# Kernel optimization log

Measured on AMD Instinct MI355X. Metric: run time of the kernel, lower is better.

The kernel has to match this reference:

```python
import jax, jax.numpy as jnp
import numpy as np
from jax.scipy.special import logsumexp

B, F, V, C, K, KP = 8192, 32, 64, 32, 8, 7  # batch, features, values/feature, classes, gate options, padded pair candidates
TEMP = 1.0
EPS = 1e-06


def _structure():
    # candidate 0 = self table; candidates 1..7 = pair tables conditioned on preceding features
    mask = np.zeros((F - 1, K), dtype=bool)
    mask[:, 0] = True
    cond = np.zeros((F - 1, KP), dtype=np.int32)
    for i in range(F - 1):
        fi = i + 1
        for j in range(min(fi, KP)):
            mask[i, j + 1] = True
            cond[i, j] = fi - 1 - j
    return jnp.asarray(cond), jnp.asarray(mask)


def setup_inputs() -> dict:
    key = jax.random.key(0)
    ks = jax.random.split(key, 6)
    cond_index, valid_mask = _structure()
    return {
        "x": jax.random.randint(ks[0], (B, F), 0, V, dtype=jnp.int32),
        "training": True,
        "class_logits": jax.random.normal(ks[1], (C,), jnp.float32) * 0.1,
        "table0": jax.random.normal(ks[2], (V, C), jnp.float32) * 0.1,
        "self_tables": jax.random.normal(ks[3], (F - 1, V, C), jnp.float32) * 0.1,
        "pair_tables": jax.random.normal(ks[4], (F - 1, KP, V, V, C), jnp.float32) * 0.1,
        "structure_logits": jax.random.normal(ks[5], (F - 1, K), jnp.float32) * 0.1,
        "u_noise": jax.random.uniform(jax.random.fold_in(key, 7), (F - 1, K), jnp.float32),
        "cond_index": cond_index,
        "valid_mask": valid_mask,
    }


def reference(x, training, class_logits, table0, self_tables, pair_tables,
              structure_logits, u_noise, cond_index, valid_mask):
    # class prior term
    cl = class_logits - logsumexp(class_logits)  # [C]
    t0 = table0 - logsumexp(table0, axis=0, keepdims=True)  # [V,C]
    out = cl[None, :] + t0[x[:, 0]]  # [B,C]

    # Gumbel-softmax gate over candidate parent sets (training path)
    g = -jnp.log(-jnp.log(u_noise + EPS) + EPS)
    gate_logits = jnp.where(valid_mask, (structure_logits + g) / TEMP, -jnp.inf)
    w = jax.nn.softmax(gate_logits, axis=-1)  # [F-1,K]; padded entries get weight 0

    f_idx = jnp.arange(F - 1)
    xs = x[:, 1:]  # [B,F-1] feature values

    # self (class-only) candidate tables, normalized over the feature-value axis
    st = self_tables - logsumexp(self_tables, axis=1, keepdims=True)  # [F-1,V,C]
    self_g = st[f_idx[None, :], xs]  # [B,F-1,C]
    out = out + jnp.einsum('bfc,f->bc', self_g, w[:, 0])

    # pair candidate tables, normalized over the feature-value axis (axis 2)
    pt = pair_tables - logsumexp(pair_tables, axis=2, keepdims=True)  # [F-1,KP,V,V,C]
    xc = x[:, cond_index]  # [B,F-1,KP] conditioning feature values
    k_idx = jnp.arange(KP)
    pair_g = pt[f_idx[None, :, None], k_idx[None, None, :], xs[:, :, None], xc]  # [B,F-1,KP,C]
    out = out + jnp.einsum('bfkc,fk->bc', pair_g, w[:, 1:])
    return out
```

## Files before the change

### kernel.cpp

```cpp
#include <hip/hip_runtime.h>
#include <math.h>

#define B_  8192
#define F_  32
#define V_  64
#define C_  32
#define KP_ 7
#define EPS_ 1e-6f

#define WS_OFF  256
#define WS_ETAB 288
#define WS_G    512
#define WS_LSE  66048

__device__ const int d_split[9] = {0, 25, 50, 74, 99, 123, 148, 172, 196};

__global__ __launch_bounds__(1024)
void prep_kernel(const float* __restrict__ cl, const float* __restrict__ t0,
                 const float* __restrict__ st, const float* __restrict__ sl,
                 const float* __restrict__ un, float* __restrict__ ws) {
    __shared__ float gl[31][8];
    __shared__ float wsm[31][8];
    __shared__ float lse_self[31][32];
    int tid = threadIdx.x;

    if (tid < 248) {
        int f = tid >> 3, k = tid & 7;
        int kmax = min(f + 1, KP_);
        bool valid = (k <= kmax);
        float u = un[tid];
        float g = -__logf(-__logf(u + EPS_) + EPS_);
        gl[f][k] = valid ? (sl[tid] + g) : -INFINITY;
    }
    if (tid >= 248 && tid < 256) ws[tid] = 0.f;
    if (tid < 200) {
        int q = tid / 25, i = tid % 25;
        int g = d_split[q] + i;
        int packed;
        if (g < d_split[q + 1]) {
            int f = 0, base = 0;
            for (;;) { int cnt = min(f + 1, KP_); if (g < base + cnt) break; base += cnt; f++; }
            int k = g - base;
            packed = ((f * 8 + k + 1) << 20) | ((f * KP_ + k) << 12) | ((f + 1) << 6) | (f - k);
        } else {
            packed = (248 << 20);
        }
        ((int*)ws)[WS_ETAB + tid] = packed;
    }
    __syncthreads();
    if (tid < 248) {
        int f = tid >> 3, k = tid & 7;
        float m = -INFINITY;
        #pragma unroll
        for (int j = 0; j < 8; j++) m = fmaxf(m, gl[f][j]);
        float s = 0.f;
        #pragma unroll
        for (int j = 0; j < 8; j++) s += __expf(gl[f][j] - m);
        float wv = __expf(gl[f][k] - m) / s;
        wsm[f][k] = wv;
        ws[tid] = wv;
    }
    if (tid < 992) {
        int f = tid >> 5, c = tid & 31;
        float s = 0.f;
        #pragma unroll 8
        for (int v = 0; v < V_; v++) s += __expf(st[(f * V_ + v) * C_ + c]);
        lse_self[f][c] = __logf(s);
    }
    __syncthreads();
    if (tid < 32) {
        int c = tid;
        float scl = 0.f;
        #pragma unroll
        for (int j = 0; j < C_; j++) scl += __expf(cl[j]);
        float lse_cl = __logf(scl);
        float s0 = 0.f;
        #pragma unroll 8
        for (int v = 0; v < V_; v++) s0 += __expf(t0[v * C_ + c]);
        float lse_t0 = __logf(s0);
        float acc = cl[c] - lse_cl - lse_t0;
        for (int f = 0; f < 31; f++) acc -= wsm[f][0] * lse_self[f][c];
        ws[WS_OFF + c] = acc;
    }
}

__global__ __launch_bounds__(256)
void lse_kernel(const float* __restrict__ pt, float* __restrict__ ws) {
    int idx = blockIdx.x * 256 + threadIdx.x;
    int c4 = idx & 7, v = (idx >> 3) & 63, fk = idx >> 9;
    const float* p = pt + (size_t)fk * (V_ * V_ * C_) + v * C_ + c4 * 4;
    float4 s = make_float4(0.f, 0.f, 0.f, 0.f);
    for (int a = 0; a < V_; a += 8) {
        float4 l[8];
        #pragma unroll
        for (int i = 0; i < 8; i++)
            l[i] = *(const float4*)(p + (a + i) * (V_ * C_));
        #pragma unroll
        for (int i = 0; i < 8; i++) {
            s.x += __expf(l[i].x); s.y += __expf(l[i].y);
            s.z += __expf(l[i].z); s.w += __expf(l[i].w);
        }
    }
    float4 r;
    r.x = __logf(s.x); r.y = __logf(s.y); r.z = __logf(s.z); r.w = __logf(s.w);
    ((float4*)(ws + WS_LSE))[idx] = r;
}

__global__ __launch_bounds__(256)
void foldg_kernel(const float* __restrict__ t0, const float* __restrict__ st,
                  float* __restrict__ ws) {
    int idx = blockIdx.x * 256 + threadIdx.x;
    int c4 = idx & 7, v = (idx >> 3) & 63, j = idx >> 9;
    int nk = min(KP_, 31 - j);
    const float4* lse4 = (const float4*)(ws + WS_LSE);
    float4 g;
    if (j == 0) {
        g = ((const float4*)t0)[v * 8 + c4];
    } else {
        float w0 = ws[(j - 1) * 8];
        float4 sv = ((const float4*)st)[((j - 1) * V_ + v) * 8 + c4];
        g.x = w0 * sv.x; g.y = w0 * sv.y; g.z = w0 * sv.z; g.w = w0 * sv.w;
    }
    for (int k = 0; k < nk; k++) {
        int f = j + k;
        float wv = ws[f * 8 + k + 1];
        float4 lv = lse4[((f * KP_ + k) * V_ + v) * 8 + c4];
        g.x -= wv * lv.x; g.y -= wv * lv.y; g.z -= wv * lv.z; g.w -= wv * lv.w;
    }
    ((float4*)(ws + WS_G))[idx] = g;
}

__global__ __launch_bounds__(256)
void main_kernel(const int* __restrict__ x, const float* __restrict__ pt,
                 const float* __restrict__ ws, float* __restrict__ out) {
    __shared__ int   xsh[4 * 33];
    __shared__ float wsh[256];
    __shared__ int   etab[200];
    __shared__ float4 offv[8];
    __shared__ float4 part[7][32];
    int tid = threadIdx.x;
    if (tid < 128) xsh[(tid >> 5) * 33 + (tid & 31)] = x[blockIdx.x * 128 + tid];
    wsh[tid] = ws[tid];
    if (tid < 200) etab[tid] = ((const int*)ws)[WS_ETAB + tid];
    if (tid < 8)   offv[tid] = ((const float4*)(ws + WS_OFF))[tid];
    __syncthreads();

    const float4* __restrict__ G4 = (const float4*)(ws + WS_G);
    int q  = tid >> 5;
    int r  = (tid >> 3) & 3;
    int c4 = tid & 7;
    const int* xrow = &xsh[r * 33];
    float4 acc = make_float4(0.f, 0.f, 0.f, 0.f);

    #pragma unroll
    for (int jj = 0; jj < 4; jj++) {
        int j = q * 4 + jj;
        float4 gv = G4[(j * V_ + xrow[j]) * 8 + c4];
        acc.x += gv.x; acc.y += gv.y; acc.z += gv.z; acc.w += gv.w;
    }
    if (q == 0) {
        float4 ov = offv[c4];
        acc.x += ov.x; acc.y += ov.y; acc.z += ov.z; acc.w += ov.w;
    }

    int beg = q * 25;
    #pragma unroll
    for (int ch = 0; ch < 5; ch++) {
        float4 pv[5];
        float  wt[5];
        #pragma unroll
        for (int i = 0; i < 5; i++) {
            int pk = etab[beg + ch * 5 + i];
            int ci = pk & 63, fi = (pk >> 6) & 63;
            int fk = (pk >> 12) & 255, widx = (pk >> 20) & 255;
            int xv = xrow[fi], xc = xrow[ci];
            pv[i] = *(const float4*)(pt + ((size_t)(fk * V_ + xv) * V_ + xc) * C_ + c4 * 4);
            wt[i] = wsh[widx];
        }
        #pragma unroll
        for (int i = 0; i < 5; i++) {
            acc.x += wt[i] * pv[i].x; acc.y += wt[i] * pv[i].y;
            acc.z += wt[i] * pv[i].z; acc.w += wt[i] * pv[i].w;
        }
    }

    if (q > 0) part[q - 1][r * 8 + c4] = acc;
    __syncthreads();
    if (q == 0) {
        #pragma unroll
        for (int p = 0; p < 7; p++) {
            float4 pv = part[p][r * 8 + c4];
            acc.x += pv.x; acc.y += pv.y; acc.z += pv.z; acc.w += pv.w;
        }
        ((float4*)out)[(blockIdx.x * 4 + r) * 8 + c4] = acc;
    }
}

extern "C" void kernel_launch(void* const* d_in, const int* in_sizes, int n_in,
                              void* d_out, int out_size, void* d_ws, size_t ws_size,
                              hipStream_t stream) {
    const int*   x   = (const int*)  d_in[0];
    const float* cl  = (const float*)d_in[2];
    const float* t0  = (const float*)d_in[3];
    const float* st  = (const float*)d_in[4];
    const float* pt  = (const float*)d_in[5];
    const float* sl  = (const float*)d_in[6];
    const float* un  = (const float*)d_in[7];
    float* ws  = (float*)d_ws;
    float* out = (float*)d_out;

    prep_kernel<<<1, 1024, 0, stream>>>(cl, t0, st, sl, un, ws);
    lse_kernel<<<434, 256, 0, stream>>>(pt, ws);
    foldg_kernel<<<64, 256, 0, stream>>>(t0, st, ws);
    main_kernel<<<2048, 256, 0, stream>>>(x, pt, ws, out);
}
```

Baseline: 230.3 us.

## Fuse prep into LSE kernel and gather pair tables from fp16 copy

Merges the single-block prep kernel into the LSE kernel as an extra block, removing one launch and the serial one-block stage. The LSE pass also writes an fp16 copy of the pair tables into workspace, and the main kernel gathers from that copy, halving bytes per random gather. The cost is an extra ~57MB write per call, and fp16 rounding of the table values adds small numerical error. The fp16 path is used only when the workspace is large enough.

```diff
diff --git a/kernel.cpp b/kernel.cpp
--- a/kernel.cpp
+++ b/kernel.cpp
@@ -1,4 +1,5 @@
 #include <hip/hip_runtime.h>
+#include <hip/hip_fp16.h>
 #include <math.h>
 
 #define B_  8192
@@ -12,98 +13,113 @@
 #define WS_ETAB 288
 #define WS_G    512
 #define WS_LSE  66048
+#define WS_H    2097152ull
+#define H_BYTES (217ull * V_ * V_ * C_ * 2ull)
+#define NEED_WS (WS_H * 4ull + H_BYTES)
 
 __device__ const int d_split[9] = {0, 25, 50, 74, 99, 123, 148, 172, 196};
 
-__global__ __launch_bounds__(1024)
-void prep_kernel(const float* __restrict__ cl, const float* __restrict__ t0,
-                 const float* __restrict__ st, const float* __restrict__ sl,
-                 const float* __restrict__ un, float* __restrict__ ws) {
-    __shared__ float gl[31][8];
-    __shared__ float wsm[31][8];
-    __shared__ float lse_self[31][32];
-    int tid = threadIdx.x;
-
-    if (tid < 248) {
-        int f = tid >> 3, k = tid & 7;
-        int kmax = min(f + 1, KP_);
-        bool valid = (k <= kmax);
-        float u = un[tid];
-        float g = -__logf(-__logf(u + EPS_) + EPS_);
-        gl[f][k] = valid ? (sl[tid] + g) : -INFINITY;
-    }
-    if (tid >= 248 && tid < 256) ws[tid] = 0.f;
-    if (tid < 200) {
-        int q = tid / 25, i = tid % 25;
-        int g = d_split[q] + i;
-        int packed;
-        if (g < d_split[q + 1]) {
-            int f = 0, base = 0;
-            for (;;) { int cnt = min(f + 1, KP_); if (g < base + cnt) break; base += cnt; f++; }
-            int k = g - base;
-            packed = ((f * 8 + k + 1) << 20) | ((f * KP_ + k) << 12) | ((f + 1) << 6) | (f - k);
+template<int CVT>
+__global__ __launch_bounds__(256)
+void lse_prep_kernel(const float* __restrict__ pt,
+                     const float* __restrict__ cl, const float* __restrict__ t0,
+                     const float* __restrict__ st, const float* __restrict__ sl,
+                     const float* __restrict__ un, float* __restrict__ ws) {
+    if (blockIdx.x < 434) {
+        int idx = blockIdx.x * 256 + threadIdx.x;
+        int c4 = idx & 7, v = (idx >> 3) & 63, fk = idx >> 9;
+        size_t eoff = (size_t)fk * (V_ * V_ * C_) + v * C_ + c4 * 4;
+        const float* p = pt + eoff;
+        __half* ph = (__half*)(ws + WS_H) + eoff;
+        float4 s = make_float4(0.f, 0.f, 0.f, 0.f);
+        for (int a = 0; a < V_; a += 8) {
+            float4 l[8];
+            #pragma unroll
+            for (int i = 0; i < 8; i++)
+                l[i] = *(const float4*)(p + (size_t)(a + i) * (V_ * C_));
+            if (CVT) {
+                #pragma unroll
+                for (int i = 0; i < 8; i++) {
+                    union { __half2 h; unsigned u; } ha, hb;
+                    ha.h = __floats2half2_rn(l[i].x, l[i].y);
+                    hb.h = __floats2half2_rn(l[i].z, l[i].w);
+                    *(uint2*)(ph + (size_t)(a + i) * (V_ * C_)) = make_uint2(ha.u, hb.u);
+                }
+            }
+            #pragma unroll
+            for (int i = 0; i < 8; i++) {
+                s.x += __expf(l[i].x); s.y += __expf(l[i].y);
+                s.z += __expf(l[i].z); s.w += __expf(l[i].w);
+            }
+        }
+        float4 r;
+        r.x = __logf(s.x); r.y = __logf(s.y); r.z = __logf(s.z); r.w = __logf(s.w);
+        ((float4*)(ws + WS_LSE))[idx] = r;
+    } else {
+        __shared__ float gl[31][8];
+        __shared__ float wsm[31][8];
+        __shared__ float lsf[31][32];
+        int tid = threadIdx.x;
+        if (tid < 248) {
+            int f = tid >> 3, k = tid & 7;
+            int kmax = min(f + 1, KP_);
+            bool valid = (k <= kmax);
+            float u = un[tid];
+            float g = -__logf(-__logf(u + EPS_) + EPS_);
+            gl[f][k] = valid ? (sl[tid] + g) : -INFINITY;
         } else {
-            packed = (248 << 20);
-        }
-        ((int*)ws)[WS_ETAB + tid] = packed;
-    }
-    __syncthreads();
-    if (tid < 248) {
-        int f = tid >> 3, k = tid & 7;
-        float m = -INFINITY;
-        #pragma unroll
-        for (int j = 0; j < 8; j++) m = fmaxf(m, gl[f][j]);
-        float s = 0.f;
-        #pragma unroll
-        for (int j = 0; j < 8; j++) s += __expf(gl[f][j] - m);
-        float wv = __expf(gl[f][k] - m) / s;
-        wsm[f][k] = wv;
-        ws[tid] = wv;
-    }
-    if (tid < 992) {
-        int f = tid >> 5, c = tid & 31;
-        float s = 0.f;
-        #pragma unroll 8
-        for (int v = 0; v < V_; v++) s += __expf(st[(f * V_ + v) * C_ + c]);
-        lse_self[f][c] = __logf(s);
-    }
-    __syncthreads();
-    if (tid < 32) {
-        int c = tid;
-        float scl = 0.f;
-        #pragma unroll
-        for (int j = 0; j < C_; j++) scl += __expf(cl[j]);
-        float lse_cl = __logf(scl);
-        float s0 = 0.f;
-        #pragma unroll 8
-        for (int v = 0; v < V_; v++) s0 += __expf(t0[v * C_ + c]);
-        float lse_t0 = __logf(s0);
-        float acc = cl[c] - lse_cl - lse_t0;
-        for (int f = 0; f < 31; f++) acc -= wsm[f][0] * lse_self[f][c];
-        ws[WS_OFF + c] = acc;
-    }
-}
-
-__global__ __launch_bounds__(256)
-void lse_kernel(const float* __restrict__ pt, float* __restrict__ ws) {
-    int idx = blockIdx.x * 256 + threadIdx.x;
-    int c4 = idx & 7, v = (idx >> 3) & 63, fk = idx >> 9;
-    const float* p = pt + (size_t)fk * (V_ * V_ * C_) + v * C_ + c4 * 4;
-    float4 s = make_float4(0.f, 0.f, 0.f, 0.f);
-    for (int a = 0; a < V_; a += 8) {
-        float4 l[8];
-        #pragma unroll
-        for (int i = 0; i < 8; i++)
-            l[i] = *(const float4*)(p + (a + i) * (V_ * C_));
-        #pragma unroll
-        for (int i = 0; i < 8; i++) {
-            s.x += __expf(l[i].x); s.y += __expf(l[i].y);
-            s.z += __expf(l[i].z); s.w += __expf(l[i].w);
-        }
-    }
-    float4 r;
-    r.x = __logf(s.x); r.y = __logf(s.y); r.z = __logf(s.z); r.w = __logf(s.w);
-    ((float4*)(ws + WS_LSE))[idx] = r;
+            ws[tid] = 0.f;
+        }
+        if (tid < 200) {
+            int q = tid / 25, i = tid % 25;
+            int g = d_split[q] + i;
+            int packed;
+            if (g < d_split[q + 1]) {
+                int f = 0, base = 0;
+                for (;;) { int cnt = min(f + 1, KP_); if (g < base + cnt) break; base += cnt; f++; }
+                int k = g - base;
+                packed = ((f * 8 + k + 1) << 20) | ((f * KP_ + k) << 12) | ((f + 1) << 6) | (f - k);
+            } else {
+                packed = (248 << 20);
+            }
+            ((int*)ws)[WS_ETAB + tid] = packed;
+        }
+        __syncthreads();
+        if (tid < 248) {
+            int f = tid >> 3, k = tid & 7;
+            float m = -INFINITY;
+            #pragma unroll
+            for (int j = 0; j < 8; j++) m = fmaxf(m, gl[f][j]);
+            float s = 0.f;
+            #pragma unroll
+            for (int j = 0; j < 8; j++) s += __expf(gl[f][j] - m);
+            float wv = __expf(gl[f][k] - m) / s;
+            wsm[f][k] = wv;
+            ws[tid] = wv;
+        }
+        for (int i = tid; i < 992; i += 256) {
+            int f = i >> 5, c = i & 31;
+            float s = 0.f;
+            #pragma unroll 8
+            for (int v = 0; v < V_; v++) s += __expf(st[(f * V_ + v) * C_ + c]);
+            lsf[f][c] = __logf(s);
+        }
+        __syncthreads();
+        if (tid < 32) {
+            int c = tid;
+            float scl = 0.f;
+            #pragma unroll
+            for (int j = 0; j < C_; j++) scl += __expf(cl[j]);
+            float lse_cl = __logf(scl);
+            float s0 = 0.f;
+            #pragma unroll 8
+            for (int v = 0; v < V_; v++) s0 += __expf(t0[v * C_ + c]);
+            float lse_t0 = __logf(s0);
+            float acc = cl[c] - lse_cl - lse_t0;
+            for (int f = 0; f < 31; f++) acc -= wsm[f][0] * lsf[f][c];
+            ws[WS_OFF + c] = acc;
+        }
+    }
 }
 
 __global__ __launch_bounds__(256)
@@ -130,6 +146,7 @@
     ((float4*)(ws + WS_G))[idx] = g;
 }
 
+template<int CVT>
 __global__ __launch_bounds__(256)
 void main_kernel(const int* __restrict__ x, const float* __restrict__ pt,
                  const float* __restrict__ ws, float* __restrict__ out) {
@@ -145,7 +162,8 @@
     if (tid < 8)   offv[tid] = ((const float4*)(ws + WS_OFF))[tid];
     __syncthreads();
 
-    const float4* __restrict__ G4 = (const float4*)(ws + WS_G);
+    const float4* __restrict__ G4  = (const float4*)(ws + WS_G);
+    const __half* __restrict__ pth = (const __half*)(ws + WS_H);
     int q  = tid >> 5;
     int r  = (tid >> 3) & 3;
     int c4 = tid & 7;
@@ -166,21 +184,44 @@
     int beg = q * 25;
     #pragma unroll
     for (int ch = 0; ch < 5; ch++) {
-        float4 pv[5];
-        float  wt[5];
-        #pragma unroll
-        for (int i = 0; i < 5; i++) {
-            int pk = etab[beg + ch * 5 + i];
-            int ci = pk & 63, fi = (pk >> 6) & 63;
-            int fk = (pk >> 12) & 255, widx = (pk >> 20) & 255;
-            int xv = xrow[fi], xc = xrow[ci];
-            pv[i] = *(const float4*)(pt + ((size_t)(fk * V_ + xv) * V_ + xc) * C_ + c4 * 4);
-            wt[i] = wsh[widx];
-        }
-        #pragma unroll
-        for (int i = 0; i < 5; i++) {
-            acc.x += wt[i] * pv[i].x; acc.y += wt[i] * pv[i].y;
-            acc.z += wt[i] * pv[i].z; acc.w += wt[i] * pv[i].w;
+        if (CVT) {
+            uint2  hv[5];
+            float  wt[5];
+            #pragma unroll
+            for (int i = 0; i < 5; i++) {
+                int pk = etab[beg + ch * 5 + i];
+                int ci = pk & 63, fi = (pk >> 6) & 63;
+                int fk = (pk >> 12) & 255, widx = (pk >> 20) & 255;
+                int xv = xrow[fi], xc = xrow[ci];
+                hv[i] = *(const uint2*)(pth + ((size_t)(fk * V_ + xv) * V_ + xc) * C_ + c4 * 4);
+                wt[i] = wsh[widx];
+            }
+            #pragma unroll
+            for (int i = 0; i < 5; i++) {
+                union { unsigned u; __half2 h; } a, b;
+                a.u = hv[i].x; b.u = hv[i].y;
+                float2 f0 = __half22float2(a.h);
+                float2 f1 = __half22float2(b.h);
+                acc.x += wt[i] * f0.x; acc.y += wt[i] * f0.y;
+                acc.z += wt[i] * f1.x; acc.w += wt[i] * f1.y;
+            }
+        } else {
+            float4 pv[5];
+            float  wt[5];
+            #pragma unroll
+            for (int i = 0; i < 5; i++) {
+                int pk = etab[beg + ch * 5 + i];
+                int ci = pk & 63, fi = (pk >> 6) & 63;
+                int fk = (pk >> 12) & 255, widx = (pk >> 20) & 255;
+                int xv = xrow[fi], xc = xrow[ci];
+                pv[i] = *(const float4*)(pt + ((size_t)(fk * V_ + xv) * V_ + xc) * C_ + c4 * 4);
+                wt[i] = wsh[widx];
+            }
+            #pragma unroll
+            for (int i = 0; i < 5; i++) {
+                acc.x += wt[i] * pv[i].x; acc.y += wt[i] * pv[i].y;
+                acc.z += wt[i] * pv[i].z; acc.w += wt[i] * pv[i].w;
+            }
         }
     }
 
@@ -209,8 +250,13 @@
     float* ws  = (float*)d_ws;
     float* out = (float*)d_out;
 
-    prep_kernel<<<1, 1024, 0, stream>>>(cl, t0, st, sl, un, ws);
-    lse_kernel<<<434, 256, 0, stream>>>(pt, ws);
-    foldg_kernel<<<64, 256, 0, stream>>>(t0, st, ws);
-    main_kernel<<<2048, 256, 0, stream>>>(x, pt, ws, out);
-}
+    if (ws_size >= NEED_WS) {
+        lse_prep_kernel<1><<<435, 256, 0, stream>>>(pt, cl, t0, st, sl, un, ws);
+        foldg_kernel<<<64, 256, 0, stream>>>(t0, st, ws);
+        main_kernel<1><<<2048, 256, 0, stream>>>(x, pt, ws, out);
+    } else {
+        lse_prep_kernel<0><<<435, 256, 0, stream>>>(pt, cl, t0, st, sl, un, ws);
+        foldg_kernel<<<64, 256, 0, stream>>>(t0, st, ws);
+        main_kernel<0><<<2048, 256, 0, stream>>>(x, pt, ws, out);
+    }
+}
```

Measured after the change: 236.7 us. 1.03x slower.

## Fuse prep into LSE kernel and split LSE reduction into two partial banks

Applied to the files above, without the earlier changes.

Merges the single-block prep kernel into the pair-table LSE kernel as an extra block, which removes one launch and lets the prep work overlap with the LSE reduction. The LSE reduction is restructured so each block handles one (f,k) table half, with threads reading contiguous float4 rows. Each half writes raw exp-sum partials to a separate workspace bank, and the fold kernel adds the two banks and takes the log. This doubles the LSE workspace traffic and shrinks prep to 256 threads, so its self-table loop now takes several passes.

```diff
diff --git a/kernel.cpp b/kernel.cpp
--- a/kernel.cpp
+++ b/kernel.cpp
@@ -12,98 +12,103 @@
 #define WS_ETAB 288
 #define WS_G    512
 #define WS_LSE  66048
+#define LSE_BANK4 111104
 
 __device__ const int d_split[9] = {0, 25, 50, 74, 99, 123, 148, 172, 196};
 
-__global__ __launch_bounds__(1024)
-void prep_kernel(const float* __restrict__ cl, const float* __restrict__ t0,
-                 const float* __restrict__ st, const float* __restrict__ sl,
-                 const float* __restrict__ un, float* __restrict__ ws) {
-    __shared__ float gl[31][8];
-    __shared__ float wsm[31][8];
-    __shared__ float lse_self[31][32];
-    int tid = threadIdx.x;
-
-    if (tid < 248) {
-        int f = tid >> 3, k = tid & 7;
-        int kmax = min(f + 1, KP_);
-        bool valid = (k <= kmax);
-        float u = un[tid];
-        float g = -__logf(-__logf(u + EPS_) + EPS_);
-        gl[f][k] = valid ? (sl[tid] + g) : -INFINITY;
-    }
-    if (tid >= 248 && tid < 256) ws[tid] = 0.f;
-    if (tid < 200) {
-        int q = tid / 25, i = tid % 25;
-        int g = d_split[q] + i;
-        int packed;
-        if (g < d_split[q + 1]) {
-            int f = 0, base = 0;
-            for (;;) { int cnt = min(f + 1, KP_); if (g < base + cnt) break; base += cnt; f++; }
-            int k = g - base;
-            packed = ((f * 8 + k + 1) << 20) | ((f * KP_ + k) << 12) | ((f + 1) << 6) | (f - k);
+__global__ __launch_bounds__(256)
+void lse_prep_kernel(const float* __restrict__ pt,
+                     const float* __restrict__ cl, const float* __restrict__ t0,
+                     const float* __restrict__ st, const float* __restrict__ sl,
+                     const float* __restrict__ un, float* __restrict__ ws) {
+    if (blockIdx.x < 434) {
+        int fk   = blockIdx.x >> 1;
+        int half = blockIdx.x & 1;
+        int t    = threadIdx.x;
+        const float4* __restrict__ p =
+            (const float4*)(pt + (size_t)fk * (V_ * V_ * C_)
+                               + (size_t)half * 32 * (V_ * C_));
+        const float4* p0 = p + t;
+        const float4* p1 = p + 256 + t;
+        float4 s0 = make_float4(0.f, 0.f, 0.f, 0.f);
+        float4 s1 = make_float4(0.f, 0.f, 0.f, 0.f);
+        #pragma unroll 4
+        for (int a = 0; a < 32; a++) {
+            float4 l0 = p0[a * 512];
+            float4 l1 = p1[a * 512];
+            s0.x += __expf(l0.x); s0.y += __expf(l0.y);
+            s0.z += __expf(l0.z); s0.w += __expf(l0.w);
+            s1.x += __expf(l1.x); s1.y += __expf(l1.y);
+            s1.z += __expf(l1.z); s1.w += __expf(l1.w);
+        }
+        float4* lseP = (float4*)(ws + WS_LSE) + (size_t)half * LSE_BANK4;
+        lseP[fk * 512 + t]       = s0;
+        lseP[fk * 512 + 256 + t] = s1;
+    } else {
+        __shared__ float gl[31][8];
+        __shared__ float wsm[31][8];
+        __shared__ float lsf[31][32];
+        int tid = threadIdx.x;
+        if (tid < 248) {
+            int f = tid >> 3, k = tid & 7;
+            int kmax = min(f + 1, KP_);
+            bool valid = (k <= kmax);
+            float u = un[tid];
+            float g = -__logf(-__logf(u + EPS_) + EPS_);
+            gl[f][k] = valid ? (sl[tid] + g) : -INFINITY;
         } else {
-            packed = (248 << 20);
-        }
-        ((int*)ws)[WS_ETAB + tid] = packed;
-    }
-    __syncthreads();
-    if (tid < 248) {
-        int f = tid >> 3, k = tid & 7;
-        float m = -INFINITY;
-        #pragma unroll
-        for (int j = 0; j < 8; j++) m = fmaxf(m, gl[f][j]);
-        float s = 0.f;
-        #pragma unroll
-        for (int j = 0; j < 8; j++) s += __expf(gl[f][j] - m);
-        float wv = __expf(gl[f][k] - m) / s;
-        wsm[f][k] = wv;
-        ws[tid] = wv;
-    }
-    if (tid < 992) {
-        int f = tid >> 5, c = tid & 31;
-        float s = 0.f;
-        #pragma unroll 8
-        for (int v = 0; v < V_; v++) s += __expf(st[(f * V_ + v) * C_ + c]);
-        lse_self[f][c] = __logf(s);
-    }
-    __syncthreads();
-    if (tid < 32) {
-        int c = tid;
-        float scl = 0.f;
-        #pragma unroll
-        for (int j = 0; j < C_; j++) scl += __expf(cl[j]);
-        float lse_cl = __logf(scl);
-        float s0 = 0.f;
-        #pragma unroll 8
-        for (int v = 0; v < V_; v++) s0 += __expf(t0[v * C_ + c]);
-        float lse_t0 = __logf(s0);
-        float acc = cl[c] - lse_cl - lse_t0;
-        for (int f = 0; f < 31; f++) acc -= wsm[f][0] * lse_self[f][c];
-        ws[WS_OFF + c] = acc;
-    }
-}
-
-__global__ __launch_bounds__(256)
-void lse_kernel(const float* __restrict__ pt, float* __restrict__ ws) {
-    int idx = blockIdx.x * 256 + threadIdx.x;
-    int c4 = idx & 7, v = (idx >> 3) & 63, fk = idx >> 9;
-    const float* p = pt + (size_t)fk * (V_ * V_ * C_) + v * C_ + c4 * 4;
-    float4 s = make_float4(0.f, 0.f, 0.f, 0.f);
-    for (int a = 0; a < V_; a += 8) {
-        float4 l[8];
-        #pragma unroll
-        for (int i = 0; i < 8; i++)
-            l[i] = *(const float4*)(p + (a + i) * (V_ * C_));
-        #pragma unroll
-        for (int i = 0; i < 8; i++) {
-            s.x += __expf(l[i].x); s.y += __expf(l[i].y);
-            s.z += __expf(l[i].z); s.w += __expf(l[i].w);
-        }
-    }
-    float4 r;
-    r.x = __logf(s.x); r.y = __logf(s.y); r.z = __logf(s.z); r.w = __logf(s.w);
-    ((float4*)(ws + WS_LSE))[idx] = r;
+            ws[tid] = 0.f;
+        }
+        if (tid < 200) {
+            int q = tid / 25, i = tid % 25;
+            int g = d_split[q] + i;
+            int packed;
+            if (g < d_split[q + 1]) {
+                int f = 0, base = 0;
+                for (;;) { int cnt = min(f + 1, KP_); if (g < base + cnt) break; base += cnt; f++; }
+                int k = g - base;
+                packed = ((f * 8 + k + 1) << 20) | ((f * KP_ + k) << 12) | ((f + 1) << 6) | (f - k);
+            } else {
+                packed = (248 << 20);
+            }
+            ((int*)ws)[WS_ETAB + tid] = packed;
+        }
+        __syncthreads();
+        if (tid < 248) {
+            int f = tid >> 3, k = tid & 7;
+            float m = -INFINITY;
+            #pragma unroll
+            for (int j = 0; j < 8; j++) m = fmaxf(m, gl[f][j]);
+            float s = 0.f;
+            #pragma unroll
+            for (int j = 0; j < 8; j++) s += __expf(gl[f][j] - m);
+            float wv = __expf(gl[f][k] - m) / s;
+            wsm[f][k] = wv;
+            ws[tid] = wv;
+        }
+        for (int i = tid; i < 992; i += 256) {
+            int f = i >> 5, c = i & 31;
+            float s = 0.f;
+            #pragma unroll 8
+            for (int v = 0; v < V_; v++) s += __expf(st[(f * V_ + v) * C_ + c]);
+            lsf[f][c] = __logf(s);
+        }
+        __syncthreads();
+        if (tid < 32) {
+            int c = tid;
+            float scl = 0.f;
+            #pragma unroll
+            for (int j = 0; j < C_; j++) scl += __expf(cl[j]);
+            float lse_cl = __logf(scl);
+            float s0 = 0.f;
+            #pragma unroll 8
+            for (int v = 0; v < V_; v++) s0 += __expf(t0[v * C_ + c]);
+            float lse_t0 = __logf(s0);
+            float acc = cl[c] - lse_cl - lse_t0;
+            for (int f = 0; f < 31; f++) acc -= wsm[f][0] * lsf[f][c];
+            ws[WS_OFF + c] = acc;
+        }
+    }
 }
 
 __global__ __launch_bounds__(256)
@@ -124,8 +129,13 @@
     for (int k = 0; k < nk; k++) {
         int f = j + k;
         float wv = ws[f * 8 + k + 1];
-        float4 lv = lse4[((f * KP_ + k) * V_ + v) * 8 + c4];
-        g.x -= wv * lv.x; g.y -= wv * lv.y; g.z -= wv * lv.z; g.w -= wv * lv.w;
+        int iq = ((f * KP_ + k) * V_ + v) * 8 + c4;
+        float4 sa = lse4[iq];
+        float4 sb = lse4[LSE_BANK4 + iq];
+        g.x -= wv * __logf(sa.x + sb.x);
+        g.y -= wv * __logf(sa.y + sb.y);
+        g.z -= wv * __logf(sa.z + sb.z);
+        g.w -= wv * __logf(sa.w + sb.w);
     }
     ((float4*)(ws + WS_G))[idx] = g;
 }
@@ -209,8 +219,7 @@
     float* ws  = (float*)d_ws;
     float* out = (float*)d_out;
 
-    prep_kernel<<<1, 1024, 0, stream>>>(cl, t0, st, sl, un, ws);
-    lse_kernel<<<434, 256, 0, stream>>>(pt, ws);
+    lse_prep_kernel<<<435, 256, 0, stream>>>(pt, cl, t0, st, sl, un, ws);
     foldg_kernel<<<64, 256, 0, stream>>>(t0, st, ws);
     main_kernel<<<2048, 256, 0, stream>>>(x, pt, ws, out);
 }
```

Result: no change. 233.6 us (+1.4%).
